# Optimization experiments

Measured on AMD Instinct MI355X. Metric: run time of the kernel, lower is better.

Reference implementation:

```python
import jax, jax.numpy as jnp
import numpy as np

NUM_STEPS = 16
FD_EPS = 1e-4  # finite-difference step used by the torch TraceEstimator


def setup_inputs() -> dict:
    key = jax.random.key(0)
    ks = jax.random.split(key, 8)
    B, D, H = 65536, 64, 256
    x = jax.random.normal(ks[0], (B, D), dtype=jnp.float32)
    eps = jax.random.normal(ks[1], (NUM_STEPS, B, D), dtype=jnp.float32)
    W0 = jax.random.normal(ks[2], (D + 1, H), dtype=jnp.float32) / np.sqrt(D + 1)
    b0 = jnp.zeros((H,), dtype=jnp.float32)
    W1 = jax.random.normal(ks[3], (H, H), dtype=jnp.float32) / np.sqrt(H)
    b1 = jnp.zeros((H,), dtype=jnp.float32)
    W2 = jax.random.normal(ks[4], (H, D), dtype=jnp.float32) / np.sqrt(H)
    b2 = jnp.zeros((D,), dtype=jnp.float32)
    return {"x": x, "eps": eps, "W0": W0, "b0": b0, "W1": W1, "b1": b1, "W2": W2, "b2": b2}


def _dynamics(t, x, W0, b0, W1, b1, W2, b2):
    # concat scalar time as an extra feature column, 2-hidden-layer ReLU MLP, residual
    tcol = jnp.full((x.shape[0], 1), t, dtype=x.dtype)
    h = jnp.concatenate([x, tcol], axis=-1)          # [B, D+1]
    h = jax.nn.relu(h @ W0 + b0)                     # [B, H]
    h = jax.nn.relu(h @ W1 + b1)                     # [B, H]
    return x + (h @ W2 + b2)                         # residual, [B, D]


def reference(x, eps, W0, b0, W1, b1, W2, b2):
    dt = 1.0 / NUM_STEPS
    f = lambda t, xx: _dynamics(t, xx, W0, b0, W1, b1, W2, b2)

    def step(carry, inputs):
        xc, ld = carry
        t, e = inputs
        # Hutchinson trace via finite-difference JVP (matches torch TraceEstimator)
        base = f(t, xc)                               # also serves as RK4 k1
        plus = f(t, xc + 0.5 * e * FD_EPS)
        jvp = (plus - base) / FD_EPS
        trace = jnp.sum(e * jvp, axis=-1)             # [B]
        ld = ld - trace * dt
        # RK4 step
        k1 = base
        k2 = f(t + dt / 2, xc + dt * k1 / 2)
        k3 = f(t + dt / 2, xc + dt * k2 / 2)
        k4 = f(t + dt, xc + dt * k3)
        xn = xc + dt * (k1 + 2 * k2 + 2 * k3 + k4) / 6
        return (xn, ld), None

    ts = jnp.arange(NUM_STEPS, dtype=x.dtype) * dt
    log_det0 = jnp.zeros((x.shape[0],), dtype=x.dtype)
    (x_out, log_det), _ = jax.lax.scan(step, (x, log_det0), (ts, eps))
    return x_out, log_det
```

## Files before the change

kernel.cpp:

```cpp
#include <hip/hip_runtime.h>

#define NSTEP 16
#define BATCH 65536
#define DD 64
#define HH 256
#define MT 64
#define H0S 264
#define ABSTR 72

typedef _Float16 half8 __attribute__((ext_vector_type(8)));
typedef float floatx4 __attribute__((ext_vector_type(4)));

__global__ __launch_bounds__(256) void prep_weights(
    const float* __restrict__ W0, const float* __restrict__ W1,
    const float* __restrict__ W2, _Float16* __restrict__ ws)
{
    int i = blockIdx.x * 256 + threadIdx.x;
    _Float16* Wt0 = ws;
    _Float16* Wt1 = ws + 16384;
    _Float16* Wt2 = ws + 16384 + 65536;
    { int n = i >> 8, k = i & 255; Wt1[i] = (_Float16)W1[k * HH + n]; }
    if (i < 16384) {
        { int n = i >> 6, k = i & 63;  Wt0[i] = (_Float16)W0[k * HH + n]; }
        { int n = i >> 8, k = i & 255; Wt2[i] = (_Float16)W2[k * DD + n]; }
    }
}

template<bool MASKED>
__device__ __forceinline__ void mlp_pass(
    const _Float16* __restrict__ Wt0, const _Float16* __restrict__ Wt1,
    const _Float16* __restrict__ Wt2,
    const float* __restrict__ b1g, const float* __restrict__ b2g,
    _Float16* h0, _Float16* h1, const _Float16* ab, const float* c0buf,
    int wave, int quad, int l16, float* outv)
{
    const floatx4 zero4 = {0.f, 0.f, 0.f, 0.f};

    floatx4 acc[4][4];
#pragma unroll
    for (int rt = 0; rt < 4; rt++)
#pragma unroll
        for (int ct = 0; ct < 4; ct++) acc[rt][ct] = zero4;
#pragma unroll
    for (int kc = 0; kc < 2; kc++) {
        half8 af[4], bf[4];
#pragma unroll
        for (int rt = 0; rt < 4; rt++)
            af[rt] = *(const half8*)(ab + (rt * 16 + l16) * ABSTR + kc * 32 + quad * 8);
#pragma unroll
        for (int ct = 0; ct < 4; ct++)
            bf[ct] = *(const half8*)(Wt0 + (wave * 64 + ct * 16 + l16) * DD + kc * 32 + quad * 8);
#pragma unroll
        for (int rt = 0; rt < 4; rt++)
#pragma unroll
            for (int ct = 0; ct < 4; ct++)
                acc[rt][ct] = __builtin_amdgcn_mfma_f32_16x16x32_f16(af[rt], bf[ct], acc[rt][ct], 0, 0, 0);
    }
#pragma unroll
    for (int ct = 0; ct < 4; ct++) {
        int col = wave * 64 + ct * 16 + l16;
        float cb = MASKED ? 0.f : c0buf[col];
#pragma unroll
        for (int rt = 0; rt < 4; rt++)
#pragma unroll
            for (int rr = 0; rr < 4; rr++) {
                int row = rt * 16 + quad * 4 + rr;
                float v = acc[rt][ct][rr];
                if (MASKED) {
                    float z = (float)h0[row * H0S + col];
                    h0[row * H0S + col] = (_Float16)(z > 0.f ? v : 0.f);
                } else {
                    v += cb;
                    h0[row * H0S + col] = (_Float16)(v > 0.f ? v : 0.f);
                }
            }
    }
    __syncthreads();

#pragma unroll
    for (int rt = 0; rt < 4; rt++)
#pragma unroll
        for (int ct = 0; ct < 4; ct++) acc[rt][ct] = zero4;
#pragma unroll
    for (int kc = 0; kc < 8; kc++) {
        half8 af[4], bf[4];
#pragma unroll
        for (int rt = 0; rt < 4; rt++)
            af[rt] = *(const half8*)(h0 + (rt * 16 + l16) * H0S + kc * 32 + quad * 8);
#pragma unroll
        for (int ct = 0; ct < 4; ct++)
            bf[ct] = *(const half8*)(Wt1 + (wave * 64 + ct * 16 + l16) * HH + kc * 32 + quad * 8);
#pragma unroll
        for (int rt = 0; rt < 4; rt++)
#pragma unroll
            for (int ct = 0; ct < 4; ct++)
                acc[rt][ct] = __builtin_amdgcn_mfma_f32_16x16x32_f16(af[rt], bf[ct], acc[rt][ct], 0, 0, 0);
    }
#pragma unroll
    for (int ct = 0; ct < 4; ct++) {
        int col = wave * 64 + ct * 16 + l16;
        float cb = MASKED ? 0.f : b1g[col];
#pragma unroll
        for (int rt = 0; rt < 4; rt++)
#pragma unroll
            for (int rr = 0; rr < 4; rr++) {
                int row = rt * 16 + quad * 4 + rr;
                float v = acc[rt][ct][rr];
                if (MASKED) {
                    float z = (float)h1[row * H0S + col];
                    h1[row * H0S + col] = (_Float16)(z > 0.f ? v : 0.f);
                } else {
                    v += cb;
                    h1[row * H0S + col] = (_Float16)(v > 0.f ? v : 0.f);
                }
            }
    }
    __syncthreads();

    floatx4 a2[4];
#pragma unroll
    for (int rt = 0; rt < 4; rt++) a2[rt] = zero4;
#pragma unroll
    for (int kc = 0; kc < 8; kc++) {
        half8 bf2 = *(const half8*)(Wt2 + (wave * 16 + l16) * HH + kc * 32 + quad * 8);
#pragma unroll
        for (int rt = 0; rt < 4; rt++) {
            half8 af = *(const half8*)(h1 + (rt * 16 + l16) * H0S + kc * 32 + quad * 8);
            a2[rt] = __builtin_amdgcn_mfma_f32_16x16x32_f16(af, bf2, a2[rt], 0, 0, 0);
        }
    }
    float bb2 = MASKED ? 0.f : b2g[wave * 16 + l16];
#pragma unroll
    for (int rt = 0; rt < 4; rt++)
#pragma unroll
        for (int rr = 0; rr < 4; rr++) outv[rt * 4 + rr] = a2[rt][rr] + bb2;
}

__global__ __launch_bounds__(256, 2) void ffjord_kernel(
    const float* __restrict__ xg, const float* __restrict__ epsg,
    const float* __restrict__ W0g, const float* __restrict__ b0g,
    const float* __restrict__ b1g, const float* __restrict__ b2g,
    const _Float16* __restrict__ ws, float* __restrict__ out)
{
    __shared__ __attribute__((aligned(16))) _Float16 h0[MT * H0S];
    __shared__ __attribute__((aligned(16))) _Float16 h1[MT * H0S];
    __shared__ __attribute__((aligned(16))) _Float16 ab[MT * ABSTR];
    __shared__ float c0buf[HH];
    __shared__ float ldacc[MT];

    const _Float16* Wt0 = ws;
    const _Float16* Wt1 = ws + 16384;
    const _Float16* Wt2 = ws + 16384 + 65536;

    const int tid  = threadIdx.x;
    const int wave = tid >> 6;
    const int lane = tid & 63;
    const int quad = lane >> 4;
    const int l16  = lane & 15;
    const int row0 = blockIdx.x * MT;
    const int colD = wave * 16 + l16;
    const float dt = 1.f / NSTEP;

    if (tid < MT) ldacc[tid] = 0.f;

    float x[16];
#pragma unroll
    for (int i = 0; i < 16; i++) {
        int r = (i >> 2) * 16 + quad * 4 + (i & 3);
        x[i] = xg[(size_t)(row0 + r) * DD + colD];
    }

#pragma unroll 1
    for (int s = 0; s < NSTEP; s++) {
        float t = s * dt;
        float e[16];
#pragma unroll
        for (int i = 0; i < 16; i++) {
            int r = (i >> 2) * 16 + quad * 4 + (i & 3);
            e[i] = epsg[(size_t)(s * BATCH + row0 + r) * DD + colD];
        }
        float xacc[16], kprev[16], yv[16], outv[16];
#pragma unroll
        for (int i = 0; i < 16; i++) { xacc[i] = x[i]; kprev[i] = 0.f; }

#pragma unroll 1
        for (int p = 0; p < 5; p++) {
            if (p == 1) {
#pragma unroll
                for (int i = 0; i < 16; i++) yv[i] = 0.5f * e[i];
#pragma unroll
                for (int i = 0; i < 16; i++) {
                    int r = (i >> 2) * 16 + quad * 4 + (i & 3);
                    ab[r * ABSTR + colD] = (_Float16)yv[i];
                }
                __syncthreads();
                mlp_pass<true>(Wt0, Wt1, Wt2, b1g, b2g, h0, h1, ab, c0buf,
                               wave, quad, l16, outv);
#pragma unroll
                for (int i = 0; i < 16; i++) {
                    float pr = e[i] * (0.5f * e[i] + outv[i]);
                    pr += __shfl_xor(pr, 1);
                    pr += __shfl_xor(pr, 2);
                    pr += __shfl_xor(pr, 4);
                    pr += __shfl_xor(pr, 8);
                    if (l16 == 0) {
                        int r = (i >> 2) * 16 + quad * 4 + (i & 3);
                        atomicAdd(&ldacc[r], -dt * pr);
                    }
                }
            } else {
                float c  = (p == 4) ? 1.f : 0.5f;
                float w  = (p == 0 || p == 4) ? dt / 6.f : dt / 3.f;
                float tp = t + ((p == 4) ? dt : (p >= 2 ? 0.5f * dt : 0.f));
#pragma unroll
                for (int i = 0; i < 16; i++) yv[i] = x[i] + c * dt * kprev[i];
#pragma unroll
                for (int i = 0; i < 16; i++) {
                    int r = (i >> 2) * 16 + quad * 4 + (i & 3);
                    ab[r * ABSTR + colD] = (_Float16)yv[i];
                }
                c0buf[tid] = tp * W0g[64 * HH + tid] + b0g[tid];
                __syncthreads();
                mlp_pass<false>(Wt0, Wt1, Wt2, b1g, b2g, h0, h1, ab, c0buf,
                                wave, quad, l16, outv);
#pragma unroll
                for (int i = 0; i < 16; i++) {
                    kprev[i] = yv[i] + outv[i];
                    xacc[i] += w * kprev[i];
                }
            }
        }
#pragma unroll
        for (int i = 0; i < 16; i++) x[i] = xacc[i];
    }

#pragma unroll
    for (int i = 0; i < 16; i++) {
        int r = (i >> 2) * 16 + quad * 4 + (i & 3);
        out[(size_t)(row0 + r) * DD + colD] = x[i];
    }
    __syncthreads();
    if (tid < MT) out[(size_t)BATCH * DD + row0 + tid] = ldacc[tid];
}

extern "C" void kernel_launch(void* const* d_in, const int* in_sizes, int n_in,
                              void* d_out, int out_size, void* d_ws, size_t ws_size,
                              hipStream_t stream) {
    const float* xg   = (const float*)d_in[0];
    const float* epsg = (const float*)d_in[1];
    const float* W0g  = (const float*)d_in[2];
    const float* b0g  = (const float*)d_in[3];
    const float* W1g  = (const float*)d_in[4];
    const float* b1g  = (const float*)d_in[5];
    const float* W2g  = (const float*)d_in[6];
    const float* b2g  = (const float*)d_in[7];
    float* outp = (float*)d_out;
    _Float16* ws = (_Float16*)d_ws;

    prep_weights<<<65536 / 256, 256, 0, stream>>>(W0g, W1g, W2g, ws);
    ffjord_kernel<<<BATCH / MT, 256, 0, stream>>>(xg, epsg, W0g, b0g, b1g, b2g, ws, outp);
}
```

Baseline: 2.950 ms.

## Hoist W0/W2 fragments and biases into registers, reload eps instead

Loads the first- and last-layer weight MFMA fragments, the biases and the time-column weight into registers once per block instead of re-reading them from global memory in every MLP pass. Stops keeping the eps values in registers across the step and reloads them from global memory where they are used, to free registers. Relaxes launch bounds from two blocks per SM to one, which gives the compiler more registers but may reduce occupancy and latency hiding.

```diff
diff --git a/kernel.cpp b/kernel.cpp
--- a/kernel.cpp
+++ b/kernel.cpp
@@ -28,9 +28,8 @@
 
 template<bool MASKED>
 __device__ __forceinline__ void mlp_pass(
-    const _Float16* __restrict__ Wt0, const _Float16* __restrict__ Wt1,
-    const _Float16* __restrict__ Wt2,
-    const float* __restrict__ b1g, const float* __restrict__ b2g,
+    const half8 (&w0f)[2][4], const _Float16* __restrict__ Wt1,
+    const half8 (&w2f)[8], const float (&b1v)[4], float bb2,
     _Float16* h0, _Float16* h1, const _Float16* ab, const float* c0buf,
     int wave, int quad, int l16, float* outv)
 {
@@ -43,18 +42,15 @@
         for (int ct = 0; ct < 4; ct++) acc[rt][ct] = zero4;
 #pragma unroll
     for (int kc = 0; kc < 2; kc++) {
-        half8 af[4], bf[4];
+        half8 af[4];
 #pragma unroll
         for (int rt = 0; rt < 4; rt++)
             af[rt] = *(const half8*)(ab + (rt * 16 + l16) * ABSTR + kc * 32 + quad * 8);
 #pragma unroll
-        for (int ct = 0; ct < 4; ct++)
-            bf[ct] = *(const half8*)(Wt0 + (wave * 64 + ct * 16 + l16) * DD + kc * 32 + quad * 8);
-#pragma unroll
         for (int rt = 0; rt < 4; rt++)
 #pragma unroll
             for (int ct = 0; ct < 4; ct++)
-                acc[rt][ct] = __builtin_amdgcn_mfma_f32_16x16x32_f16(af[rt], bf[ct], acc[rt][ct], 0, 0, 0);
+                acc[rt][ct] = __builtin_amdgcn_mfma_f32_16x16x32_f16(af[rt], w0f[kc][ct], acc[rt][ct], 0, 0, 0);
     }
 #pragma unroll
     for (int ct = 0; ct < 4; ct++) {
@@ -99,7 +95,7 @@
 #pragma unroll
     for (int ct = 0; ct < 4; ct++) {
         int col = wave * 64 + ct * 16 + l16;
-        float cb = MASKED ? 0.f : b1g[col];
+        float cb = MASKED ? 0.f : b1v[ct];
 #pragma unroll
         for (int rt = 0; rt < 4; rt++)
 #pragma unroll
@@ -122,21 +118,20 @@
     for (int rt = 0; rt < 4; rt++) a2[rt] = zero4;
 #pragma unroll
     for (int kc = 0; kc < 8; kc++) {
-        half8 bf2 = *(const half8*)(Wt2 + (wave * 16 + l16) * HH + kc * 32 + quad * 8);
 #pragma unroll
         for (int rt = 0; rt < 4; rt++) {
             half8 af = *(const half8*)(h1 + (rt * 16 + l16) * H0S + kc * 32 + quad * 8);
-            a2[rt] = __builtin_amdgcn_mfma_f32_16x16x32_f16(af, bf2, a2[rt], 0, 0, 0);
+            a2[rt] = __builtin_amdgcn_mfma_f32_16x16x32_f16(af, w2f[kc], a2[rt], 0, 0, 0);
         }
     }
-    float bb2 = MASKED ? 0.f : b2g[wave * 16 + l16];
+    float bb = MASKED ? 0.f : bb2;
 #pragma unroll
     for (int rt = 0; rt < 4; rt++)
 #pragma unroll
-        for (int rr = 0; rr < 4; rr++) outv[rt * 4 + rr] = a2[rt][rr] + bb2;
-}
-
-__global__ __launch_bounds__(256, 2) void ffjord_kernel(
+        for (int rr = 0; rr < 4; rr++) outv[rt * 4 + rr] = a2[rt][rr] + bb;
+}
+
+__global__ __launch_bounds__(256, 1) void ffjord_kernel(
     const float* __restrict__ xg, const float* __restrict__ epsg,
     const float* __restrict__ W0g, const float* __restrict__ b0g,
     const float* __restrict__ b1g, const float* __restrict__ b2g,
@@ -163,6 +158,23 @@
 
     if (tid < MT) ldacc[tid] = 0.f;
 
+    half8 w0f[2][4];
+#pragma unroll
+    for (int kc = 0; kc < 2; kc++)
+#pragma unroll
+        for (int ct = 0; ct < 4; ct++)
+            w0f[kc][ct] = *(const half8*)(Wt0 + (wave * 64 + ct * 16 + l16) * DD + kc * 32 + quad * 8);
+    half8 w2f[8];
+#pragma unroll
+    for (int kc = 0; kc < 8; kc++)
+        w2f[kc] = *(const half8*)(Wt2 + (wave * 16 + l16) * HH + kc * 32 + quad * 8);
+    float b1v[4];
+#pragma unroll
+    for (int ct = 0; ct < 4; ct++) b1v[ct] = b1g[wave * 64 + ct * 16 + l16];
+    const float bb2 = b2g[wave * 16 + l16];
+    const float w0t = W0g[64 * HH + tid];
+    const float b0v = b0g[tid];
+
     float x[16];
 #pragma unroll
     for (int i = 0; i < 16; i++) {
@@ -173,13 +185,7 @@
 #pragma unroll 1
     for (int s = 0; s < NSTEP; s++) {
         float t = s * dt;
-        float e[16];
-#pragma unroll
-        for (int i = 0; i < 16; i++) {
-            int r = (i >> 2) * 16 + quad * 4 + (i & 3);
-            e[i] = epsg[(size_t)(s * BATCH + row0 + r) * DD + colD];
-        }
-        float xacc[16], kprev[16], yv[16], outv[16];
+        float xacc[16], kprev[16], outv[16];
 #pragma unroll
         for (int i = 0; i < 16; i++) { xacc[i] = x[i]; kprev[i] = 0.f; }
 
@@ -187,45 +193,41 @@
         for (int p = 0; p < 5; p++) {
             if (p == 1) {
 #pragma unroll
-                for (int i = 0; i < 16; i++) yv[i] = 0.5f * e[i];
-#pragma unroll
                 for (int i = 0; i < 16; i++) {
                     int r = (i >> 2) * 16 + quad * 4 + (i & 3);
-                    ab[r * ABSTR + colD] = (_Float16)yv[i];
+                    float ev = epsg[(size_t)(s * BATCH + row0 + r) * DD + colD];
+                    ab[r * ABSTR + colD] = (_Float16)(0.5f * ev);
                 }
                 __syncthreads();
-                mlp_pass<true>(Wt0, Wt1, Wt2, b1g, b2g, h0, h1, ab, c0buf,
+                mlp_pass<true>(w0f, Wt1, w2f, b1v, bb2, h0, h1, ab, c0buf,
                                wave, quad, l16, outv);
 #pragma unroll
                 for (int i = 0; i < 16; i++) {
-                    float pr = e[i] * (0.5f * e[i] + outv[i]);
+                    int r = (i >> 2) * 16 + quad * 4 + (i & 3);
+                    float ev = epsg[(size_t)(s * BATCH + row0 + r) * DD + colD];
+                    float pr = ev * (0.5f * ev + outv[i]);
                     pr += __shfl_xor(pr, 1);
                     pr += __shfl_xor(pr, 2);
                     pr += __shfl_xor(pr, 4);
                     pr += __shfl_xor(pr, 8);
-                    if (l16 == 0) {
-                        int r = (i >> 2) * 16 + quad * 4 + (i & 3);
-                        atomicAdd(&ldacc[r], -dt * pr);
-                    }
+                    if (l16 == 0) atomicAdd(&ldacc[r], -dt * pr);
                 }
             } else {
                 float c  = (p == 4) ? 1.f : 0.5f;
                 float w  = (p == 0 || p == 4) ? dt / 6.f : dt / 3.f;
                 float tp = t + ((p == 4) ? dt : (p >= 2 ? 0.5f * dt : 0.f));
 #pragma unroll
-                for (int i = 0; i < 16; i++) yv[i] = x[i] + c * dt * kprev[i];
-#pragma unroll
                 for (int i = 0; i < 16; i++) {
                     int r = (i >> 2) * 16 + quad * 4 + (i & 3);
-                    ab[r * ABSTR + colD] = (_Float16)yv[i];
-                }
-                c0buf[tid] = tp * W0g[64 * HH + tid] + b0g[tid];
+                    ab[r * ABSTR + colD] = (_Float16)(x[i] + c * dt * kprev[i]);
+                }
+                c0buf[tid] = tp * w0t + b0v;
                 __syncthreads();
-                mlp_pass<false>(Wt0, Wt1, Wt2, b1g, b2g, h0, h1, ab, c0buf,
+                mlp_pass<false>(w0f, Wt1, w2f, b1v, bb2, h0, h1, ab, c0buf,
                                 wave, quad, l16, outv);
 #pragma unroll
                 for (int i = 0; i < 16; i++) {
-                    kprev[i] = yv[i] + outv[i];
+                    kprev[i] = x[i] + c * dt * kprev[i] + outv[i];
                     xacc[i] += w * kprev[i];
                 }
             }
```

Result: faster. 2.733 ms (-7.4%).
